# Kernel tuning notes

Hardware: AMD Instinct MI355X
Metric: run time of the kernel (lower is better)

Reference implementation:

```python
import jax, jax.numpy as jnp
import numpy as np

# --- stochastic-computing constants (match FSUMGUCell defaults) ---
BW_W = 8                      # FSULinearPC weight bitstream bitwidth
BW_M = 4                      # FSUMul bitwidth (shift-register depth)
DEPTH = 10                    # FSUAdd accumulator depth
ACC_MAX = 2.0 ** (DEPTH - 2)  # +256
ACC_MIN = -ACC_MAX
NW = 2 ** BW_W
NM = 2 ** BW_M
# deterministic pseudo-random comparison sequences (stand-in for UnarySim Sobol RNG)
_RNG_W = jnp.asarray(np.random.RandomState(0).permutation(NW), dtype=jnp.float32)
_RNG_WI = jnp.asarray(np.random.RandomState(1).permutation(NW), dtype=jnp.float32)
_RNG_M = jnp.asarray(np.random.RandomState(2).permutation(NM), dtype=jnp.float32)


def _fsu_add(acc, s, offset, scale):
    # FSUAdd (bipolar): accumulate (parallel count - offset), clamp, emit bit when acc >= scale
    acc = jnp.clip(acc + s - offset, ACC_MIN, ACC_MAX)
    out = (acc >= scale).astype(jnp.float32)
    return acc - out * scale, out


def _linear_pc(x_aug, w_src, t):
    # FSULinearPC (bipolar): weight bits generated by rate coding (source > rng[t]),
    # XNOR with input bits, summed into a parallel count. x_aug: [B, F+1] (bias col of 1s).
    wb_p = (w_src > _RNG_W[t % NW]).astype(jnp.float32)   # [O, F+1]
    wb_i = (w_src > _RNG_WI[t % NW]).astype(jnp.float32)
    return x_aug @ wb_p.T + (1.0 - x_aug) @ (1.0 - wb_i).T


def _fsu_mul(state, in0, in1):
    # FSUMul non-static bipolar: estimate P(in1) with a BW_M-bit shift register,
    # regenerate a bit via rng comparison; XNOR-style pos/inv paths gated by in0,
    # with conditionally-advanced rng indices (enable-signal semantics).
    sr, idx_p, idx_i = state
    sr = jnp.concatenate([sr[1:], in1[None]], axis=0)      # shift in newest bit
    cnt = sr.sum(0) * (NM / BW_M)                          # scale count to rng range
    bit_p = (cnt > _RNG_M[idx_p % NM]).astype(jnp.float32)
    bit_i = (cnt > _RNG_M[idx_i % NM]).astype(jnp.float32)
    out = in0 * bit_p + (1.0 - in0) * (1.0 - bit_i)        # disjoint paths -> OR == +
    idx_p = idx_p + in0.astype(jnp.int32)
    idx_i = idx_i + (1 - in0.astype(jnp.int32))
    return (sr, idx_p, idx_i), out


def _w_src(w, b):
    # SourceGen bipolar: binary value in [-1,1] -> integer source in [0, 2^BW_W]
    aug = jnp.concatenate([w, b[:, None]], axis=1)
    return jnp.round((jnp.clip(aug, -1.0, 1.0) + 1.0) * 0.5 * NW)


def _forward(x_bits, hx0, weight_ih, bias_ih, weight_hh, bias_hh):
    T, B, I = x_bits.shape
    H = hx0.shape[1]
    src_ih = _w_src(weight_ih, bias_ih)   # [2H, I+1]
    src_hh = _w_src(weight_hh, bias_hh)   # [2H, H+1]
    ones_col = jnp.ones((B, 1), jnp.float32)
    acc0 = jnp.zeros((B, H), jnp.float32)
    sr0 = jnp.tile((jnp.arange(BW_M) % 2).astype(jnp.float32)[:, None, None], (1, B, H))
    mul0 = (sr0, jnp.zeros((B, H), jnp.int32), jnp.zeros((B, H), jnp.int32))
    off_fg = (I + H + 2 - 1) / 2.0        # entry=I+H+2, scaled=False -> scale=1

    def step(carry, xt):
        h, a1, a2, a3, a4, a5, a6, m1, m2, m3, t = carry
        gate_i = _linear_pc(jnp.concatenate([xt, ones_col], 1), src_ih, t)  # [B, 2H]
        gate_h = _linear_pc(jnp.concatenate([h, ones_col], 1), src_hh, t)
        i_f, i_n = gate_i[:, :H], gate_i[:, H:]
        h_f, h_n = gate_h[:, :H], gate_h[:, H:]
        a1, fg_in = _fsu_add(a1, i_f + h_f, off_fg, 1.0)
        a2, fg = _fsu_add(a2, fg_in + 1.0, 0.0, 2.0)          # scaled (x+1)/2 hardsigmoid
        a3, h_n_bit = _fsu_add(a3, h_n, H / 2.0, 1.0)          # entry=H+1
        m1, ng_prod = _fsu_mul(m1, fg, h_n_bit)
        a4, i_n_bit = _fsu_add(a4, i_n, I / 2.0, 1.0)          # entry=I+1
        a5, ng = _fsu_add(a5, i_n_bit + ng_prod, 0.5, 1.0)     # entry=2
        m2, fgi_prod = _fsu_mul(m2, 1.0 - fg, ng)
        m3, fg_prod = _fsu_mul(m3, fg, h)
        a6, hy = _fsu_add(a6, ng + fgi_prod + fg_prod, 1.0, 1.0)  # entry=3
        return (hy, a1, a2, a3, a4, a5, a6, m1, m2, m3, t + 1), hy

    carry0 = (hx0, acc0, acc0, acc0, acc0, acc0, acc0, mul0, mul0, mul0, jnp.int32(0))
    _, hy_stream = jax.lax.scan(step, carry0, x_bits)
    return hy_stream  # [T, B, H] unary bitstream of hidden state


def setup_inputs():
    key = jax.random.key(0)
    ks = jax.random.split(key, 6)
    T, B, I, H = 64, 128, 1024, 1024
    x_bits = jax.random.bernoulli(ks[0], 0.5, (T, B, I)).astype(jnp.float32)
    hx0 = jax.random.bernoulli(ks[1], 0.5, (B, H)).astype(jnp.float32)
    weight_ih = jax.random.uniform(ks[2], (2 * H, I), jnp.float32, -1.0, 1.0)
    bias_ih = jax.random.uniform(ks[3], (2 * H,), jnp.float32, -1.0, 1.0)
    weight_hh = jax.random.uniform(ks[4], (2 * H, H), jnp.float32, -1.0, 1.0)
    bias_hh = jax.random.uniform(ks[5], (2 * H,), jnp.float32, -1.0, 1.0)
    return {"x_bits": x_bits, "hx0": hx0, "weight_ih": weight_ih, "bias_ih": bias_ih,
            "weight_hh": weight_hh, "bias_hh": bias_hh}


def reference(x_bits, hx0, weight_ih, bias_ih, weight_hh, bias_hh):
    return _forward(x_bits, hx0, weight_ih, bias_ih, weight_hh, bias_hh)
```

## Files before the change

### kernel.cpp

```cpp
#include <hip/hip_runtime.h>


#define NBLK 256
#define NTHR 512

#define WS_BAR_SUB   0u
#define WS_BAR_MST   1024u
#define WS_BAR_FLG   2048u
#define WS_RNGW   8192u
#define WS_RNGWI  9216u
#define WS_RNGM   10240u
#define WS_SRCB   12288u
#define WS_SRCW   20480u
#define WS_XP     8409088u
#define WS_HW     9457664u
#define WS_DT     9523200u
#define WS_MASKS  10571776u

struct SRng {
  unsigned mt[3][624];
  unsigned yb[3][624];
  unsigned draws[3][1248];
  int perm[3][256];
};
struct SC {
  unsigned short rows[16][1028];
  int rngw[64];
  int rngwi[64];
};
struct SL {
  unsigned long long mask2[2][64*34];
  unsigned xb[32*34];
  unsigned short hrow16[32*68];
  int rngm[16];
};
union SU { SRng r; SC c; SL l; };

__device__ __forceinline__ unsigned mt_temper(unsigned y){
  y ^= y >> 11;
  y ^= (y << 7)  & 0x9d2c5680u;
  y ^= (y << 15) & 0xefc60000u;
  y ^= y >> 18;
  return y;
}

__device__ void mt_regen_serial(unsigned* mt){
  for (int i = 0; i < 624; i++){
    unsigned y = (mt[i] & 0x80000000u) | (mt[(i+1)%624] & 0x7fffffffu);
    mt[i] = mt[(i+397)%624] ^ (y >> 1) ^ ((y & 1u) ? 0x9908b0dfu : 0u);
  }
}

__device__ void rng_gen(SU* sm, int* rngw, int* rngwi, int* rngm){
  const int tid = threadIdx.x;
  const int wv = tid >> 6, lane = tid & 63;
  const bool act = (wv < 3);
  if (act && lane == 0){
    unsigned* mt = sm->r.mt[wv];
    mt[0] = (unsigned)wv;
    for (int i = 1; i < 624; i++)
      mt[i] = 1812433253u * (mt[i-1] ^ (mt[i-1] >> 30)) + (unsigned)i;
  }
  __syncthreads();
  for (int r = 0; r < 2; r++){
    if (act){
      unsigned* mt = sm->r.mt[wv]; unsigned* yb = sm->r.yb[wv];
      for (int i = lane; i < 623; i += 64)
        yb[i] = (mt[i] & 0x80000000u) | (mt[i+1] & 0x7fffffffu);
    }
    __syncthreads();
    if (act){
      unsigned* mt = sm->r.mt[wv]; unsigned* yb = sm->r.yb[wv];
      for (int i = lane; i < 227; i += 64){
        unsigned y = yb[i];
        mt[i] = mt[i+397] ^ (y >> 1) ^ ((y & 1u) ? 0x9908b0dfu : 0u);
      }
    }
    __syncthreads();
    if (act){
      unsigned* mt = sm->r.mt[wv]; unsigned* yb = sm->r.yb[wv];
      for (int i = 227 + lane; i < 454; i += 64){
        unsigned y = yb[i];
        mt[i] = mt[i-227] ^ (y >> 1) ^ ((y & 1u) ? 0x9908b0dfu : 0u);
      }
    }
    __syncthreads();
    if (act){
      unsigned* mt = sm->r.mt[wv]; unsigned* yb = sm->r.yb[wv];
      for (int i = 454 + lane; i < 624; i += 64){
        unsigned y = (i < 623) ? yb[i]
                   : ((mt[623] & 0x80000000u) | (mt[0] & 0x7fffffffu));
        mt[i] = mt[i-227] ^ (y >> 1) ^ ((y & 1u) ? 0x9908b0dfu : 0u);
      }
    }
    __syncthreads();
    if (act){
      unsigned* mt = sm->r.mt[wv];
      for (int i = lane; i < 624; i += 64)
        sm->r.draws[wv][r*624 + i] = mt_temper(mt[i]);
    }
    __syncthreads();
  }
  if (act && lane == 0){
    const int n = (wv == 2) ? 16 : 256;
    int* perm = sm->r.perm[wv];
    for (int i = 0; i < n; i++) perm[i] = i;
    int dp = 0, spos = 624;
    unsigned* mt = sm->r.mt[wv];
    for (int i = n - 1; i > 0; i--){
      unsigned mask = (unsigned)i;
      mask |= mask >> 1; mask |= mask >> 2; mask |= mask >> 4;
      mask |= mask >> 8; mask |= mask >> 16;
      unsigned v;
      do {
        unsigned d;
        if (dp < 1248) d = sm->r.draws[wv][dp++];
        else {
          if (spos >= 624){ mt_regen_serial(mt); spos = 0; }
          d = mt_temper(mt[spos++]);
        }
        v = d & mask;
      } while (v > (unsigned)i);
      int tmp = perm[i]; perm[i] = perm[v]; perm[v] = tmp;
    }
    int* dst = (wv == 0) ? rngw : (wv == 1) ? rngwi : rngm;
    for (int i = 0; i < n; i++) dst[i] = perm[i];
  }
}

__device__ __forceinline__ void gbar_full(unsigned char* ws, unsigned ep){
  __syncthreads();
  if (threadIdx.x == 0){
    __threadfence();
    unsigned* sub = (unsigned*)(ws + WS_BAR_SUB + (blockIdx.x & 7)*128);
    unsigned old = atomicAdd(sub, 1u);
    if (old == ep*32u - 1u){
      unsigned* mst = (unsigned*)(ws + WS_BAR_MST);
      unsigned mo = atomicAdd(mst, 1u);
      if (mo == ep*8u - 1u){
        for (int i = 0; i < 8; i++)
          __hip_atomic_store((unsigned*)(ws + WS_BAR_FLG + i*128), ep,
                             __ATOMIC_RELAXED, __HIP_MEMORY_SCOPE_AGENT);
      }
    }
    const unsigned* fl = (const unsigned*)(ws + WS_BAR_FLG + (blockIdx.x & 7)*128);
    while (__hip_atomic_load(fl, __ATOMIC_RELAXED, __HIP_MEMORY_SCOPE_AGENT) < ep)
      __builtin_amdgcn_s_sleep(8);
  }
  __syncthreads();
  __threadfence();
}

__device__ __forceinline__ int clampi(int v){
  v = v < -512 ? -512 : v;
  v = v >  512 ?  512 : v;
  return v;
}

__global__ void __launch_bounds__(NTHR)
fsu_kernel(const float* __restrict__ x, const float* __restrict__ hx0,
           const float* __restrict__ wih, const float* __restrict__ bih,
           const float* __restrict__ whh, const float* __restrict__ bhh,
           float* __restrict__ out, unsigned char* __restrict__ ws)
{
  __shared__ SU sm;
  const int tid = threadIdx.x;
  const int bid = blockIdx.x;

  int* rngw  = (int*)(ws + WS_RNGW);
  int* rngwi = (int*)(ws + WS_RNGWI);
  int* rngm  = (int*)(ws + WS_RNGM);
  unsigned short* srcb = (unsigned short*)(ws + WS_SRCB);
  unsigned short* srcw = (unsigned short*)(ws + WS_SRCW);
  unsigned* xp   = (unsigned*)(ws + WS_XP);
  unsigned long long* hw = (unsigned long long*)(ws + WS_HW);
  int* Dt = (int*)(ws + WS_DT);
  unsigned long long* masks = (unsigned long long*)(ws + WS_MASKS);

  if (bid == 0){
    rng_gen(&sm, rngw, rngwi, rngm);
  } else {
    const int gtid = (bid - 1)*NTHR + tid;
    const int lane = tid & 63;
    const int gw = gtid >> 6;
    const int nw = (NBLK-1)*(NTHR/64);
    const int nthr = (NBLK-1)*NTHR;
    for (int ch = gw; ch < 131072; ch += nw){
      float v = x[(size_t)ch*64 + lane];
      unsigned long long bal = __ballot(v != 0.0f);
      if ((lane & 31) == 0) xp[ch*2 + (lane >> 5)] = (unsigned)(bal >> lane);
    }
    for (int idx = gtid; idx < 4096; idx += nthr){
      int bg2 = idx >> 10, jt2 = (idx >> 4) & 63, rp2 = idx & 15;
      int r0 = bg2*32 + 2*rp2;
      unsigned v = 0;
      for (int j = 0; j < 16; j++){
        v |= (hx0[(size_t)r0*1024 + jt2*16 + j] != 0.0f) ? (1u<<j) : 0u;
        v |= (hx0[(size_t)(r0+1)*1024 + jt2*16 + j] != 0.0f) ? (1u<<(16+j)) : 0u;
      }
      hw[idx] = (unsigned long long)v;
    }
    for (int idx = gtid; idx < 4096*1024; idx += nthr){
      int c = idx >> 10, k = idx & 1023;
      float wv2 = (c < 2048) ? wih[(size_t)c*1024 + k] : whh[(size_t)(c - 2048)*1024 + k];
      float cl = fminf(fmaxf(wv2, -1.0f), 1.0f);
      srcw[idx] = (unsigned short)(int)rintf((cl + 1.0f)*0.5f*256.0f);
    }
    for (int c = gtid; c < 4096; c += nthr){
      float bv = (c < 2048) ? bih[c] : bhh[c - 2048];
      float cl = fminf(fmaxf(bv, -1.0f), 1.0f);
      srcb[c] = (unsigned short)(int)rintf((cl + 1.0f)*0.5f*256.0f);
    }
  }
  gbar_full(ws, 1u);

  {
    const int c0 = bid * 16;
    const unsigned* srcw32 = (const unsigned*)srcw;
    for (int q = tid; q < 16*512; q += NTHR){
      int r = q >> 9, w = q & 511;
      ((unsigned*)&sm.c.rows[r][0])[w] = srcw32[(size_t)(c0 + r)*512 + w];
    }
    if (tid < 64) sm.c.rngw[tid] = rngw[tid];
    if (tid >= 64 && tid < 128) sm.c.rngwi[tid - 64] = rngwi[tid - 64];
    __syncthreads();
    for (int rr = 0; rr < 2; rr++){
      int row = tid + rr*NTHR;
      int t = row >> 4, lc = row & 15, col = c0 + lc;
      int rp = sm.c.rngw[t], ri = sm.c.rngwi[t];
      int hi = rp > ri ? rp : ri;
      int lo1 = (rp < ri ? rp : ri) + 1;
      bool rihi = (ri >= rp);
      const unsigned* srow = (const unsigned*)&sm.c.rows[lc][0];
      unsigned long long* gdst = masks + ((size_t)t*4096 + col)*32;
      int cnti = 0;
      for (int w = 0; w < 32; w++){
        unsigned pos = 0, neg = 0;
        #pragma unroll
        for (int i2 = 15; i2 >= 0; i2--){
          unsigned v2 = srow[w*16 + i2];
          int vH = (int)(v2 >> 16);
          int vL = (int)(v2 & 0xFFFFu);
          pos = (pos << 1) | ((unsigned)(hi - vH) >> 31);
          neg = (neg << 1) | ((unsigned)(vH - lo1) >> 31);
          pos = (pos << 1) | ((unsigned)(hi - vL) >> 31);
          neg = (neg << 1) | ((unsigned)(vL - lo1) >> 31);
        }
        gdst[w] = (unsigned long long)pos | ((unsigned long long)neg << 32);
        cnti += rihi ? __popc(pos) : (32 - __popc(neg));
      }
      Dt[t*4096 + col] = 1024 - cnti + (((int)srcb[col] > rp) ? 1 : 0);
    }
  }
  gbar_full(ws, 2u);

  const int jt = bid & 63, bg = bid >> 6;
  const int j0 = jt * 16, b0 = bg * 32;
  const int b_l = tid >> 4, j_l = tid & 15;
  const int bglob = b0 + b_l;

  int hcur = (hx0[(size_t)bglob*1024 + j0 + j_l] != 0.0f) ? 1 : 0;
  int A1=0,A2=0,A3=0,A4=0,A5=0,A6=0;
  unsigned sr1=10u, sr2=10u, sr3=10u;
  int i1p=0,i1i=0,i2p=0,i2i=0,i3p=0,i3i=0;

  if (tid < 16) sm.l.rngm[tid] = rngm[tid];

  const unsigned* msrc = (const unsigned*)masks;
  int cur = 0;
  int xgf, xgn, dhf, dhn;
  unsigned mreg[8], xreg[2];
  int dreg[4];

  {
    unsigned* mbuf = (unsigned*)sm.l.mask2[0];
    #pragma unroll
    for (int i = 0; i < 8; i++){
      int q = tid + i*NTHR;
      int r = q >> 6, qq = q & 63;
      int c = (r >> 4)*1024 + j0 + (r & 15);
      mbuf[r*68 + qq] = msrc[((size_t)0*4096 + c)*64 + qq];
    }
    #pragma unroll
    for (int i = 0; i < 2; i++){
      int q = tid + i*NTHR;
      int bb = q >> 5, w = q & 31;
      sm.l.xb[bb*34 + w] = xp[((size_t)0*128 + b0 + bb)*32 + w];
    }
    #pragma unroll
    for (int i = 0; i < 2; i++){
      int q = tid + i*NTHR;
      unsigned long long v = __hip_atomic_load(&hw[(size_t)bg*1024 + q],
                                               __ATOMIC_RELAXED,
                                               __HIP_MEMORY_SCOPE_AGENT);
      int jt_ = q >> 4, rp_ = q & 15;
      unsigned data = (unsigned)v;
      sm.l.hrow16[(2*rp_)*68 + jt_]   = (unsigned short)(data & 0xFFFFu);
      sm.l.hrow16[(2*rp_+1)*68 + jt_] = (unsigned short)(data >> 16);
    }
    int d0[4];
    #pragma unroll
    for (int g = 0; g < 4; g++) d0[g] = Dt[0*4096 + g*1024 + j0 + j_l];
    __syncthreads();
    int p0=0,n0=0,p1=0,n1=0;
    const uint2* xrow = (const uint2*)&sm.l.xb[b_l*34];
    const ulonglong2* m0p = (const ulonglong2*)&sm.l.mask2[0][(0  + j_l)*34];
    const ulonglong2* m1p = (const ulonglong2*)&sm.l.mask2[0][(16 + j_l)*34];
    #pragma unroll
    for (int w2 = 0; w2 < 16; w2++){
      uint2 xv = xrow[w2];
      ulonglong2 a = m0p[w2];
      p0 += __popc(xv.x & (unsigned)a.x) + __popc(xv.y & (unsigned)a.y);
      n0 += __popc(xv.x & (unsigned)(a.x >> 32)) + __popc(xv.y & (unsigned)(a.y >> 32));
      ulonglong2 b = m1p[w2];
      p1 += __popc(xv.x & (unsigned)b.x) + __popc(xv.y & (unsigned)b.y);
      n1 += __popc(xv.x & (unsigned)(b.x >> 32)) + __popc(xv.y & (unsigned)(b.y >> 32));
    }
    xgf = d0[0] + p0 - n0;
    xgn = d0[1] + p1 - n1;
    dhf = d0[2]; dhn = d0[3];
    #pragma unroll
    for (int i = 0; i < 8; i++){
      int q = tid + i*NTHR;
      int r = q >> 6, qq = q & 63;
      int c = (r >> 4)*1024 + j0 + (r & 15);
      mreg[i] = msrc[((size_t)1*4096 + c)*64 + qq];
    }
    #pragma unroll
    for (int i = 0; i < 2; i++){
      int q = tid + i*NTHR;
      int bb = q >> 5, w = q & 31;
      xreg[i] = xp[((size_t)1*128 + b0 + bb)*32 + w];
    }
    #pragma unroll
    for (int g = 0; g < 4; g++) dreg[g] = Dt[1*4096 + g*1024 + j0 + j_l];
  }

  for (int t = 0; t < 64; t++){
    const int par = t & 1;

    int p2=0,n2=0,p3=0,n3=0;
    {
      const uint2* hrow = (const uint2*)&sm.l.hrow16[b_l*68];
      const ulonglong2* m2p = (const ulonglong2*)&sm.l.mask2[cur][(32 + j_l)*34];
      const ulonglong2* m3p = (const ulonglong2*)&sm.l.mask2[cur][(48 + j_l)*34];
      #pragma unroll
      for (int w2 = 0; w2 < 16; w2++){
        uint2 hv = hrow[w2];
        ulonglong2 c2 = m2p[w2];
        p2 += __popc(hv.x & (unsigned)c2.x) + __popc(hv.y & (unsigned)c2.y);
        n2 += __popc(hv.x & (unsigned)(c2.x >> 32)) + __popc(hv.y & (unsigned)(c2.y >> 32));
        ulonglong2 d = m3p[w2];
        p3 += __popc(hv.x & (unsigned)d.x) + __popc(hv.y & (unsigned)d.y);
        n3 += __popc(hv.x & (unsigned)(d.x >> 32)) + __popc(hv.y & (unsigned)(d.y >> 32));
      }
    }
    const int g_hf = dhf + p2 - n2;
    const int g_hn = dhn + p3 - n3;

    int s1 = xgf + g_hf;
    A1 = clampi(A1 + 2*s1 - 2049);
    int fg_in = (A1 >= 2); A1 -= fg_in << 1;
    A2 = clampi(A2 + ((fg_in + 1) << 1));
    int fg = (A2 >= 4); A2 -= fg << 2;
    A3 = clampi(A3 + (g_hn << 1) - 1024);
    int hnb = (A3 >= 2); A3 -= hnb << 1;

    sr1 = ((sr1 >> 1) | ((unsigned)hnb << 3)) & 0xFu;
    int ng_prod;
    {
      int cv = __popc(sr1) << 2;
      int bp = cv > sm.l.rngm[i1p & 15];
      int bi = cv > sm.l.rngm[i1i & 15];
      ng_prod = fg ? bp : (1 - bi);
      i1p += fg; i1i += 1 - fg;
    }
    A4 = clampi(A4 + (xgn << 1) - 1024);
    int inb = (A4 >= 2); A4 -= inb << 1;
    A5 = clampi(A5 + ((inb + ng_prod) << 1) - 1);
    int ng = (A5 >= 2); A5 -= ng << 1;

    sr2 = ((sr2 >> 1) | ((unsigned)ng << 3)) & 0xFu;
    int fgi;
    {
      int cv = __popc(sr2) << 2;
      int bp = cv > sm.l.rngm[i2p & 15];
      int bi = cv > sm.l.rngm[i2i & 15];
      fgi = (1 - fg) ? bp : (1 - bi);
      i2p += 1 - fg; i2i += fg;
    }
    sr3 = ((sr3 >> 1) | ((unsigned)hcur << 3)) & 0xFu;
    int fgp;
    {
      int cv = __popc(sr3) << 2;
      int bp = cv > sm.l.rngm[i3p & 15];
      int bi = cv > sm.l.rngm[i3i & 15];
      fgp = fg ? bp : (1 - bi);
      i3p += fg; i3i += 1 - fg;
    }
    A6 = clampi(A6 + ((ng + fgi + fgp) << 1) - 2);
    int hy = (A6 >= 2); A6 -= hy << 1;
    hcur = hy;

    if (t < 63){
      unsigned long long bal = __ballot(hy);
      if ((tid & 31) == 0){
        unsigned data = (unsigned)(bal >> (tid & 32));
        unsigned long long val = (unsigned long long)data
                               | ((unsigned long long)(unsigned)(t + 1) << 32);
        __hip_atomic_store(
            &hw[(((size_t)((par ^ 1)*4 + bg))*64 + jt)*16 + (tid >> 5)], val,
            __ATOMIC_RELAXED, __HIP_MEMORY_SCOPE_AGENT);
      }
    }
    out[(size_t)t*131072 + (size_t)bglob*1024 + j0 + j_l] = (float)hy;

    if (t < 63){
      {
        unsigned* mbuf = (unsigned*)sm.l.mask2[cur ^ 1];
        #pragma unroll
        for (int i = 0; i < 8; i++){
          int q = tid + i*NTHR;
          int r = q >> 6, qq = q & 63;
          mbuf[r*68 + qq] = mreg[i];
        }
        #pragma unroll
        for (int i = 0; i < 2; i++){
          int q = tid + i*NTHR;
          int bb = q >> 5, w = q & 31;
          sm.l.xb[bb*34 + w] = xreg[i];
        }
      }
      __syncthreads();

      {
        int p0=0,n0=0,p1=0,n1=0;
        const uint2* xrow = (const uint2*)&sm.l.xb[b_l*34];
        const ulonglong2* m0p = (const ulonglong2*)&sm.l.mask2[cur ^ 1][(0  + j_l)*34];
        const ulonglong2* m1p = (const ulonglong2*)&sm.l.mask2[cur ^ 1][(16 + j_l)*34];
        #pragma unroll
        for (int w2 = 0; w2 < 16; w2++){
          uint2 xv = xrow[w2];
          ulonglong2 a = m0p[w2];
          p0 += __popc(xv.x & (unsigned)a.x) + __popc(xv.y & (unsigned)a.y);
          n0 += __popc(xv.x & (unsigned)(a.x >> 32)) + __popc(xv.y & (unsigned)(a.y >> 32));
          ulonglong2 b = m1p[w2];
          p1 += __popc(xv.x & (unsigned)b.x) + __popc(xv.y & (unsigned)b.y);
          n1 += __popc(xv.x & (unsigned)(b.x >> 32)) + __popc(xv.y & (unsigned)(b.y >> 32));
        }
        xgf = dreg[0] + p0 - n0;
        xgn = dreg[1] + p1 - n1;
        dhf = dreg[2]; dhn = dreg[3];
      }

      if (t < 62){
        #pragma unroll
        for (int i = 0; i < 8; i++){
          int q = tid + i*NTHR;
          int r = q >> 6, qq = q & 63;
          int c = (r >> 4)*1024 + j0 + (r & 15);
          mreg[i] = msrc[((size_t)(t+2)*4096 + c)*64 + qq];
        }
        #pragma unroll
        for (int i = 0; i < 2; i++){
          int q = tid + i*NTHR;
          int bb = q >> 5, w = q & 31;
          xreg[i] = xp[((size_t)(t+2)*128 + b0 + bb)*32 + w];
        }
        #pragma unroll
        for (int g = 0; g < 4; g++)
          dreg[g] = Dt[(t+2)*4096 + g*1024 + j0 + j_l];
      }

      {
        const unsigned ep = (unsigned)(t + 1);
        #pragma unroll
        for (int i = 0; i < 2; i++){
          int q = tid + i*NTHR;
          const unsigned long long* slot =
              &hw[((size_t)((par ^ 1)*4 + bg))*1024 + q];
          unsigned long long v = __hip_atomic_load(slot, __ATOMIC_RELAXED,
                                                   __HIP_MEMORY_SCOPE_AGENT);
          while ((unsigned)(v >> 32) < ep){
            __builtin_amdgcn_s_sleep(1);
            v = __hip_atomic_load(slot, __ATOMIC_RELAXED,
                                  __HIP_MEMORY_SCOPE_AGENT);
          }
          int jt_ = q >> 4, rp_ = q & 15;
          unsigned data = (unsigned)v;
          sm.l.hrow16[(2*rp_)*68 + jt_]   = (unsigned short)(data & 0xFFFFu);
          sm.l.hrow16[(2*rp_+1)*68 + jt_] = (unsigned short)(data >> 16);
        }
      }
      __syncthreads();
      cur ^= 1;
    }
  }
}

extern "C" void kernel_launch(void* const* d_in, const int* in_sizes, int n_in,
                              void* d_out, int out_size, void* d_ws, size_t ws_size,
                              hipStream_t stream)
{
  (void)in_sizes; (void)n_in; (void)out_size; (void)ws_size;
  const float* x   = (const float*)d_in[0];
  const float* hx0 = (const float*)d_in[1];
  const float* wih = (const float*)d_in[2];
  const float* bih = (const float*)d_in[3];
  const float* whh = (const float*)d_in[4];
  const float* bhh = (const float*)d_in[5];
  float* out = (float*)d_out;
  unsigned char* ws = (unsigned char*)d_ws;

  hipMemsetAsync(d_ws, 0, 4096, stream);
  hipMemsetAsync(ws + WS_HW, 0, 65536, stream);

  void* args[] = { (void*)&x, (void*)&hx0, (void*)&wih, (void*)&bih,
                   (void*)&whh, (void*)&bhh, (void*)&out, (void*)&ws };
  hipLaunchCooperativeKernel(reinterpret_cast<void*>(fsu_kernel),
                             dim3(NBLK), dim3(NTHR), args, 0, stream);
}
```

Measured before the change: 497.7 us.

## Double threads per block, split popcount K-range across half-waves with bitfield-select

Raises the block to 1024 threads so that two threads share each (batch, hidden) output. Each thread handles half of the 16 popcount words, and the two halves are combined with a cross-lane shuffle. The positive/negative popcount pairs are merged into a single popcount of a bit-select, and the negative-mask count is folded into the precomputed Dt offset to keep the maths equivalent. The aim is to shorten the per-step serial popcount chain in the latency-bound recurrent loop, at the cost of more threads per CU, higher barrier cost, and a changed ballot/hidden-state packing layout.

```diff
diff --git a/kernel.cpp b/kernel.cpp
--- a/kernel.cpp
+++ b/kernel.cpp
@@ -2,7 +2,7 @@
 
 
 #define NBLK 256
-#define NTHR 512
+#define NTHR 1024
 
 #define WS_BAR_SUB   0u
 #define WS_BAR_MST   1024u
@@ -157,6 +157,10 @@
   return v;
 }
 
+__device__ __forceinline__ unsigned bfi(unsigned x, unsigned p, unsigned n){
+  return (x & p) | (~x & n);
+}
+
 __global__ void __launch_bounds__(NTHR)
 fsu_kernel(const float* __restrict__ x, const float* __restrict__ hx0,
            const float* __restrict__ wih, const float* __restrict__ bih,
@@ -224,8 +228,7 @@
     if (tid < 64) sm.c.rngw[tid] = rngw[tid];
     if (tid >= 64 && tid < 128) sm.c.rngwi[tid - 64] = rngwi[tid - 64];
     __syncthreads();
-    for (int rr = 0; rr < 2; rr++){
-      int row = tid + rr*NTHR;
+    for (int row = tid; row < 1024; row += NTHR){
       int t = row >> 4, lc = row & 15, col = c0 + lc;
       int rp = sm.c.rngw[t], ri = sm.c.rngwi[t];
       int hi = rp > ri ? rp : ri;
@@ -233,7 +236,7 @@
       bool rihi = (ri >= rp);
       const unsigned* srow = (const unsigned*)&sm.c.rows[lc][0];
       unsigned long long* gdst = masks + ((size_t)t*4096 + col)*32;
-      int cnti = 0;
+      int cnti = 0, cntn = 0;
       for (int w = 0; w < 32; w++){
         unsigned pos = 0, neg = 0;
         #pragma unroll
@@ -248,16 +251,20 @@
         }
         gdst[w] = (unsigned long long)pos | ((unsigned long long)neg << 32);
         cnti += rihi ? __popc(pos) : (32 - __popc(neg));
-      }
-      Dt[t*4096 + col] = 1024 - cnti + (((int)srcb[col] > rp) ? 1 : 0);
+        cntn += __popc(neg);
+      }
+      Dt[t*4096 + col] = 1024 - cnti - cntn + (((int)srcb[col] > rp) ? 1 : 0);
     }
   }
   gbar_full(ws, 2u);
 
   const int jt = bid & 63, bg = bid >> 6;
   const int j0 = jt * 16, b0 = bg * 32;
-  const int b_l = tid >> 4, j_l = tid & 15;
+  const int kh  = (tid >> 5) & 1;
+  const int o   = ((tid >> 6) << 5) + (tid & 31);
+  const int b_l = o >> 4, j_l = o & 15;
   const int bglob = b0 + b_l;
+  const int w2lo = kh << 3;
 
   int hcur = (hx0[(size_t)bglob*1024 + j0 + j_l] != 0.0f) ? 1 : 0;
   int A1=0,A2=0,A3=0,A4=0,A5=0,A6=0;
@@ -269,68 +276,64 @@
   const unsigned* msrc = (const unsigned*)masks;
   int cur = 0;
   int xgf, xgn, dhf, dhn;
-  unsigned mreg[8], xreg[2];
+  unsigned mreg[4], xreg;
   int dreg[4];
 
   {
     unsigned* mbuf = (unsigned*)sm.l.mask2[0];
     #pragma unroll
-    for (int i = 0; i < 8; i++){
+    for (int i = 0; i < 4; i++){
       int q = tid + i*NTHR;
       int r = q >> 6, qq = q & 63;
       int c = (r >> 4)*1024 + j0 + (r & 15);
       mbuf[r*68 + qq] = msrc[((size_t)0*4096 + c)*64 + qq];
     }
-    #pragma unroll
-    for (int i = 0; i < 2; i++){
-      int q = tid + i*NTHR;
-      int bb = q >> 5, w = q & 31;
+    {
+      int bb = tid >> 5, w = tid & 31;
       sm.l.xb[bb*34 + w] = xp[((size_t)0*128 + b0 + bb)*32 + w];
     }
-    #pragma unroll
-    for (int i = 0; i < 2; i++){
-      int q = tid + i*NTHR;
-      unsigned long long v = __hip_atomic_load(&hw[(size_t)bg*1024 + q],
+    {
+      unsigned long long v = __hip_atomic_load(&hw[(size_t)bg*1024 + tid],
                                                __ATOMIC_RELAXED,
                                                __HIP_MEMORY_SCOPE_AGENT);
-      int jt_ = q >> 4, rp_ = q & 15;
+      int jt_ = tid >> 4, rp_ = tid & 15;
       unsigned data = (unsigned)v;
       sm.l.hrow16[(2*rp_)*68 + jt_]   = (unsigned short)(data & 0xFFFFu);
       sm.l.hrow16[(2*rp_+1)*68 + jt_] = (unsigned short)(data >> 16);
     }
-    int d0[4];
     #pragma unroll
-    for (int g = 0; g < 4; g++) d0[g] = Dt[0*4096 + g*1024 + j0 + j_l];
-    __syncthreads();
-    int p0=0,n0=0,p1=0,n1=0;
+    for (int g = 0; g < 4; g++) dreg[g] = Dt[0*4096 + g*1024 + j0 + j_l];
+    __syncthreads();
+    int s0=0, s1=0;
     const uint2* xrow = (const uint2*)&sm.l.xb[b_l*34];
     const ulonglong2* m0p = (const ulonglong2*)&sm.l.mask2[0][(0  + j_l)*34];
     const ulonglong2* m1p = (const ulonglong2*)&sm.l.mask2[0][(16 + j_l)*34];
     #pragma unroll
-    for (int w2 = 0; w2 < 16; w2++){
+    for (int w2i = 0; w2i < 8; w2i++){
+      int w2 = w2lo + w2i;
       uint2 xv = xrow[w2];
       ulonglong2 a = m0p[w2];
-      p0 += __popc(xv.x & (unsigned)a.x) + __popc(xv.y & (unsigned)a.y);
-      n0 += __popc(xv.x & (unsigned)(a.x >> 32)) + __popc(xv.y & (unsigned)(a.y >> 32));
+      s0 += __popc(bfi(xv.x, (unsigned)a.x, (unsigned)(a.x >> 32)));
+      s0 += __popc(bfi(xv.y, (unsigned)a.y, (unsigned)(a.y >> 32)));
       ulonglong2 b = m1p[w2];
-      p1 += __popc(xv.x & (unsigned)b.x) + __popc(xv.y & (unsigned)b.y);
-      n1 += __popc(xv.x & (unsigned)(b.x >> 32)) + __popc(xv.y & (unsigned)(b.y >> 32));
-    }
-    xgf = d0[0] + p0 - n0;
-    xgn = d0[1] + p1 - n1;
-    dhf = d0[2]; dhn = d0[3];
+      s1 += __popc(bfi(xv.x, (unsigned)b.x, (unsigned)(b.x >> 32)));
+      s1 += __popc(bfi(xv.y, (unsigned)b.y, (unsigned)(b.y >> 32)));
+    }
+    s0 += __shfl_xor(s0, 32);
+    s1 += __shfl_xor(s1, 32);
+    xgf = dreg[0] + s0;
+    xgn = dreg[1] + s1;
+    dhf = dreg[2]; dhn = dreg[3];
     #pragma unroll
-    for (int i = 0; i < 8; i++){
+    for (int i = 0; i < 4; i++){
       int q = tid + i*NTHR;
       int r = q >> 6, qq = q & 63;
       int c = (r >> 4)*1024 + j0 + (r & 15);
       mreg[i] = msrc[((size_t)1*4096 + c)*64 + qq];
     }
-    #pragma unroll
-    for (int i = 0; i < 2; i++){
-      int q = tid + i*NTHR;
-      int bb = q >> 5, w = q & 31;
-      xreg[i] = xp[((size_t)1*128 + b0 + bb)*32 + w];
+    {
+      int bb = tid >> 5, w = tid & 31;
+      xreg = xp[((size_t)1*128 + b0 + bb)*32 + w];
     }
     #pragma unroll
     for (int g = 0; g < 4; g++) dreg[g] = Dt[1*4096 + g*1024 + j0 + j_l];
@@ -339,27 +342,30 @@
   for (int t = 0; t < 64; t++){
     const int par = t & 1;
 
-    int p2=0,n2=0,p3=0,n3=0;
+    int s2=0, s3=0;
     {
       const uint2* hrow = (const uint2*)&sm.l.hrow16[b_l*68];
       const ulonglong2* m2p = (const ulonglong2*)&sm.l.mask2[cur][(32 + j_l)*34];
       const ulonglong2* m3p = (const ulonglong2*)&sm.l.mask2[cur][(48 + j_l)*34];
       #pragma unroll
-      for (int w2 = 0; w2 < 16; w2++){
+      for (int w2i = 0; w2i < 8; w2i++){
+        int w2 = w2lo + w2i;
         uint2 hv = hrow[w2];
         ulonglong2 c2 = m2p[w2];
-        p2 += __popc(hv.x & (unsigned)c2.x) + __popc(hv.y & (unsigned)c2.y);
-        n2 += __popc(hv.x & (unsigned)(c2.x >> 32)) + __popc(hv.y & (unsigned)(c2.y >> 32));
+        s2 += __popc(bfi(hv.x, (unsigned)c2.x, (unsigned)(c2.x >> 32)));
+        s2 += __popc(bfi(hv.y, (unsigned)c2.y, (unsigned)(c2.y >> 32)));
         ulonglong2 d = m3p[w2];
-        p3 += __popc(hv.x & (unsigned)d.x) + __popc(hv.y & (unsigned)d.y);
-        n3 += __popc(hv.x & (unsigned)(d.x >> 32)) + __popc(hv.y & (unsigned)(d.y >> 32));
-      }
-    }
-    const int g_hf = dhf + p2 - n2;
-    const int g_hn = dhn + p3 - n3;
-
-    int s1 = xgf + g_hf;
-    A1 = clampi(A1 + 2*s1 - 2049);
+        s3 += __popc(bfi(hv.x, (unsigned)d.x, (unsigned)(d.x >> 32)));
+        s3 += __popc(bfi(hv.y, (unsigned)d.y, (unsigned)(d.y >> 32)));
+      }
+    }
+    s2 += __shfl_xor(s2, 32);
+    s3 += __shfl_xor(s3, 32);
+    const int g_hf = dhf + s2;
+    const int g_hn = dhn + s3;
+
+    int s1v = xgf + g_hf;
+    A1 = clampi(A1 + 2*s1v - 2049);
     int fg_in = (A1 >= 2); A1 -= fg_in << 1;
     A2 = clampi(A2 + ((fg_in + 1) << 1));
     int fg = (A2 >= 4); A2 -= fg << 2;
@@ -404,97 +410,90 @@
 
     if (t < 63){
       unsigned long long bal = __ballot(hy);
-      if ((tid & 31) == 0){
-        unsigned data = (unsigned)(bal >> (tid & 32));
+      if ((tid & 63) == 0){
+        unsigned data = (unsigned)bal;
         unsigned long long val = (unsigned long long)data
                                | ((unsigned long long)(unsigned)(t + 1) << 32);
         __hip_atomic_store(
-            &hw[(((size_t)((par ^ 1)*4 + bg))*64 + jt)*16 + (tid >> 5)], val,
+            &hw[(((size_t)((par ^ 1)*4 + bg))*64 + jt)*16 + (tid >> 6)], val,
             __ATOMIC_RELAXED, __HIP_MEMORY_SCOPE_AGENT);
       }
     }
-    out[(size_t)t*131072 + (size_t)bglob*1024 + j0 + j_l] = (float)hy;
-
-    if (t < 63){
+    if (kh == 0)
+      out[(size_t)t*131072 + (size_t)bglob*1024 + j0 + j_l] = (float)hy;
+    if (t == 63) break;
+
+    {
+      unsigned* mbuf = (unsigned*)sm.l.mask2[cur ^ 1];
+      #pragma unroll
+      for (int i = 0; i < 4; i++){
+        int q = tid + i*NTHR;
+        int r = q >> 6, qq = q & 63;
+        mbuf[r*68 + qq] = mreg[i];
+      }
+      int bb = tid >> 5, w = tid & 31;
+      sm.l.xb[bb*34 + w] = xreg;
+    }
+    __syncthreads();
+
+    {
+      int s0=0, s1b=0;
+      const uint2* xrow = (const uint2*)&sm.l.xb[b_l*34];
+      const ulonglong2* m0p = (const ulonglong2*)&sm.l.mask2[cur ^ 1][(0  + j_l)*34];
+      const ulonglong2* m1p = (const ulonglong2*)&sm.l.mask2[cur ^ 1][(16 + j_l)*34];
+      #pragma unroll
+      for (int w2i = 0; w2i < 8; w2i++){
+        int w2 = w2lo + w2i;
+        uint2 xv = xrow[w2];
+        ulonglong2 a = m0p[w2];
+        s0 += __popc(bfi(xv.x, (unsigned)a.x, (unsigned)(a.x >> 32)));
+        s0 += __popc(bfi(xv.y, (unsigned)a.y, (unsigned)(a.y >> 32)));
+        ulonglong2 b = m1p[w2];
+        s1b += __popc(bfi(xv.x, (unsigned)b.x, (unsigned)(b.x >> 32)));
+        s1b += __popc(bfi(xv.y, (unsigned)b.y, (unsigned)(b.y >> 32)));
+      }
+      s0 += __shfl_xor(s0, 32);
+      s1b += __shfl_xor(s1b, 32);
+      xgf = dreg[0] + s0;
+      xgn = dreg[1] + s1b;
+      dhf = dreg[2]; dhn = dreg[3];
+    }
+
+    if (t < 62){
+      #pragma unroll
+      for (int i = 0; i < 4; i++){
+        int q = tid + i*NTHR;
+        int r = q >> 6, qq = q & 63;
+        int c = (r >> 4)*1024 + j0 + (r & 15);
+        mreg[i] = msrc[((size_t)(t+2)*4096 + c)*64 + qq];
+      }
       {
-        unsigned* mbuf = (unsigned*)sm.l.mask2[cur ^ 1];
-        #pragma unroll
-        for (int i = 0; i < 8; i++){
-          int q = tid + i*NTHR;
-          int r = q >> 6, qq = q & 63;
-          mbuf[r*68 + qq] = mreg[i];
-        }
-        #pragma unroll
-        for (int i = 0; i < 2; i++){
-          int q = tid + i*NTHR;
-          int bb = q >> 5, w = q & 31;
-          sm.l.xb[bb*34 + w] = xreg[i];
-        }
-      }
-      __syncthreads();
-
-      {
-        int p0=0,n0=0,p1=0,n1=0;
-        const uint2* xrow = (const uint2*)&sm.l.xb[b_l*34];
-        const ulonglong2* m0p = (const ulonglong2*)&sm.l.mask2[cur ^ 1][(0  + j_l)*34];
-        const ulonglong2* m1p = (const ulonglong2*)&sm.l.mask2[cur ^ 1][(16 + j_l)*34];
-        #pragma unroll
-        for (int w2 = 0; w2 < 16; w2++){
-          uint2 xv = xrow[w2];
-          ulonglong2 a = m0p[w2];
-          p0 += __popc(xv.x & (unsigned)a.x) + __popc(xv.y & (unsigned)a.y);
-          n0 += __popc(xv.x & (unsigned)(a.x >> 32)) + __popc(xv.y & (unsigned)(a.y >> 32));
-          ulonglong2 b = m1p[w2];
-          p1 += __popc(xv.x & (unsigned)b.x) + __popc(xv.y & (unsigned)b.y);
-          n1 += __popc(xv.x & (unsigned)(b.x >> 32)) + __popc(xv.y & (unsigned)(b.y >> 32));
-        }
-        xgf = dreg[0] + p0 - n0;
-        xgn = dreg[1] + p1 - n1;
-        dhf = dreg[2]; dhn = dreg[3];
-      }
-
-      if (t < 62){
-        #pragma unroll
-        for (int i = 0; i < 8; i++){
-          int q = tid + i*NTHR;
-          int r = q >> 6, qq = q & 63;
-          int c = (r >> 4)*1024 + j0 + (r & 15);
-          mreg[i] = msrc[((size_t)(t+2)*4096 + c)*64 + qq];
-        }
-        #pragma unroll
-        for (int i = 0; i < 2; i++){
-          int q = tid + i*NTHR;
-          int bb = q >> 5, w = q & 31;
-          xreg[i] = xp[((size_t)(t+2)*128 + b0 + bb)*32 + w];
-        }
-        #pragma unroll
-        for (int g = 0; g < 4; g++)
-          dreg[g] = Dt[(t+2)*4096 + g*1024 + j0 + j_l];
-      }
-
-      {
-        const unsigned ep = (unsigned)(t + 1);
-        #pragma unroll
-        for (int i = 0; i < 2; i++){
-          int q = tid + i*NTHR;
-          const unsigned long long* slot =
-              &hw[((size_t)((par ^ 1)*4 + bg))*1024 + q];
-          unsigned long long v = __hip_atomic_load(slot, __ATOMIC_RELAXED,
-                                                   __HIP_MEMORY_SCOPE_AGENT);
-          while ((unsigned)(v >> 32) < ep){
-            __builtin_amdgcn_s_sleep(1);
-            v = __hip_atomic_load(slot, __ATOMIC_RELAXED,
-                                  __HIP_MEMORY_SCOPE_AGENT);
-          }
-          int jt_ = q >> 4, rp_ = q & 15;
-          unsigned data = (unsigned)v;
-          sm.l.hrow16[(2*rp_)*68 + jt_]   = (unsigned short)(data & 0xFFFFu);
-          sm.l.hrow16[(2*rp_+1)*68 + jt_] = (unsigned short)(data >> 16);
-        }
-      }
-      __syncthreads();
-      cur ^= 1;
-    }
+        int bb = tid >> 5, w = tid & 31;
+        xreg = xp[((size_t)(t+2)*128 + b0 + bb)*32 + w];
+      }
+      #pragma unroll
+      for (int g = 0; g < 4; g++)
+        dreg[g] = Dt[(t+2)*4096 + g*1024 + j0 + j_l];
+    }
+
+    {
+      const unsigned ep = (unsigned)(t + 1);
+      const unsigned long long* slot =
+          &hw[((size_t)((par ^ 1)*4 + bg))*1024 + tid];
+      unsigned long long v = __hip_atomic_load(slot, __ATOMIC_RELAXED,
+                                               __HIP_MEMORY_SCOPE_AGENT);
+      while ((unsigned)(v >> 32) < ep){
+        __builtin_amdgcn_s_sleep(1);
+        v = __hip_atomic_load(slot, __ATOMIC_RELAXED,
+                              __HIP_MEMORY_SCOPE_AGENT);
+      }
+      int jt_ = tid >> 4, rp_ = tid & 15;
+      unsigned data = (unsigned)v;
+      sm.l.hrow16[(2*rp_)*68 + jt_]   = (unsigned short)(data & 0xFFFFu);
+      sm.l.hrow16[(2*rp_+1)*68 + jt_] = (unsigned short)(data >> 16);
+    }
+    __syncthreads();
+    cur ^= 1;
   }
 }
 
```

New measurement: 481.2 us. 3.3% less time.
